# Kernel optimization log

Hardware: AMD Instinct MI355X
Metric: run time of the kernel (lower is better)

Reference implementation:

```python
import jax, jax.numpy as jnp
import numpy as np

NUM_HEADS = 8


def _cross_attn(q, k, v, mask, scale):
    # q: [N,H,Dh], k/v: [M,H,Dh], mask: [N,M] bool (True = same graph)
    scores = jnp.einsum('nhd,mhd->hnm', q, k) * scale          # [H,N,M]
    scores = jnp.where(mask[None, :, :], scores, jnp.float32(-1e9))
    attn = jax.nn.softmax(scores, axis=-1)                      # [H,N,M]
    return jnp.einsum('hnm,mhd->nhd', attn, v)                  # [N,H,Dh]


def setup_inputs() -> dict:
    key = jax.random.key(0)
    ks = jax.random.split(key, 12)
    Nd, Nr, Dd, Dr, Hd, B = 2048, 4096, 128, 128, 256, 64
    drug_nodes = jax.random.normal(ks[0], (Nd, Dd), jnp.float32)
    rna_nodes = jax.random.normal(ks[1], (Nr, Dr), jnp.float32)
    drug_batch_idx = jnp.sort(jax.random.randint(ks[2], (Nd,), 0, B, dtype=jnp.int32))
    rna_batch_idx = jnp.sort(jax.random.randint(ks[3], (Nr,), 0, B, dtype=jnp.int32))
    def lin(k, fan_in, fan_out):
        bound = 1.0 / np.sqrt(fan_in)
        return jax.random.uniform(k, (fan_in, fan_out), jnp.float32, -bound, bound)
    Wq_d = lin(ks[4], Dd, Hd)
    Wk_r = lin(ks[5], Dr, Hd)
    Wv_r = lin(ks[6], Dr, Hd)
    Wo_d = lin(ks[7], Hd, Dd)
    bo_d = jnp.zeros((Dd,), jnp.float32)
    Wq_r = lin(ks[8], Dr, Hd)
    Wk_d = lin(ks[9], Dd, Hd)
    Wv_d = lin(ks[10], Dd, Hd)
    Wo_r = lin(ks[11], Hd, Dr)
    bo_r = jnp.zeros((Dr,), jnp.float32)
    return dict(drug_nodes=drug_nodes, rna_nodes=rna_nodes,
                Wq_d=Wq_d, Wk_r=Wk_r, Wv_r=Wv_r, Wo_d=Wo_d, bo_d=bo_d,
                Wq_r=Wq_r, Wk_d=Wk_d, Wv_d=Wv_d, Wo_r=Wo_r, bo_r=bo_r,
                drug_batch_idx=drug_batch_idx, rna_batch_idx=rna_batch_idx)


def reference(drug_nodes, rna_nodes, Wq_d, Wk_r, Wv_r, Wo_d, bo_d,
              Wq_r, Wk_d, Wv_d, Wo_r, bo_r, drug_batch_idx, rna_batch_idx):
    H = NUM_HEADS
    Nd, Nr = drug_nodes.shape[0], rna_nodes.shape[0]
    head_dim = Wq_d.shape[1] // H
    scale = jnp.float32(head_dim) ** -0.5
    # block-diagonal batch mask: True where drug atom and RNA node share a graph
    mask = drug_batch_idx[:, None] == rna_batch_idx[None, :]   # [Nd, Nr]

    # drug queries attend to RNA keys/values
    q_d = (drug_nodes @ Wq_d).reshape(Nd, H, head_dim)
    k_r = (rna_nodes @ Wk_r).reshape(Nr, H, head_dim)
    v_r = (rna_nodes @ Wv_r).reshape(Nr, H, head_dim)
    ctx_drug = _cross_attn(q_d, k_r, v_r, mask, scale).reshape(Nd, H * head_dim)
    ctx_drug = ctx_drug @ Wo_d + bo_d                           # [Nd, drug_dim]

    # RNA queries attend to drug keys/values
    q_r = (rna_nodes @ Wq_r).reshape(Nr, H, head_dim)
    k_d = (drug_nodes @ Wk_d).reshape(Nd, H, head_dim)
    v_d = (drug_nodes @ Wv_d).reshape(Nd, H, head_dim)
    ctx_rna = _cross_attn(q_r, k_d, v_d, mask.T, scale).reshape(Nr, H * head_dim)
    ctx_rna = ctx_rna @ Wo_r + bo_r                             # [Nr, rna_dim]

    return (ctx_drug, ctx_rna)
```

## Files before the change

kernel.cpp:

```cpp
#include <hip/hip_runtime.h>
#include <math.h>

#define NHEADS 8
#define DH 32
#define NB 64
#define PR 8
#define OPR 8
#define KT 112

__global__ __launch_bounds__(256) void proj_all(
    const float* __restrict__ Xd, const float* __restrict__ Xr,
    int Nd, int Nr, float scale,
    const float* __restrict__ Wq_d, const float* __restrict__ Wk_d, const float* __restrict__ Wv_d,
    const float* __restrict__ Wq_r, const float* __restrict__ Wk_r, const float* __restrict__ Wv_r,
    float* __restrict__ Qd, float* __restrict__ Kd, float* __restrict__ Vd,
    float* __restrict__ Qr, float* __restrict__ Kr, float* __restrict__ Vr,
    const int* __restrict__ didx, const int* __restrict__ ridx,
    int* __restrict__ dstart, int* __restrict__ rstart)
{
    int t = threadIdx.x;
    if (blockIdx.x == 0) {
        if (t <= NB) {
            int lo = 0, hi = Nd;
            while (lo < hi) { int mid = (lo + hi) >> 1; if (didx[mid] < t) lo = mid + 1; else hi = mid; }
            dstart[t] = lo;
        } else if (t >= 128 && t <= 128 + NB) {
            int v = t - 128, lo = 0, hi = Nr;
            while (lo < hi) { int mid = (lo + hi) >> 1; if (ridx[mid] < v) lo = mid + 1; else hi = mid; }
            rstart[v] = lo;
        }
    }

    int ndc = Nd / PR;
    int chunk = blockIdx.x;
    const float *X, *Wq, *Wk, *Wv;
    float *Q, *K, *V;
    int N, row0;
    if (chunk < ndc) {
        X = Xd; N = Nd; row0 = chunk * PR;
        Wq = Wq_d; Wk = Wk_d; Wv = Wv_d; Q = Qd; K = Kd; V = Vd;
    } else {
        X = Xr; N = Nr; row0 = (chunk - ndc) * PR;
        Wq = Wq_r; Wk = Wk_r; Wv = Wv_r; Q = Qr; K = Kr; V = Vr;
    }

    __shared__ float xs[PR][128];
    ((float4*)xs)[t] = ((const float4*)(X + (size_t)row0 * 128))[t];
    __syncthreads();

    float aq[PR], ak[PR], av[PR];
#pragma unroll
    for (int r = 0; r < PR; ++r) { aq[r] = 0.f; ak[r] = 0.f; av[r] = 0.f; }

    for (int k = 0; k < 128; ++k) {
        float wq = Wq[k * 256 + t];
        float wk = Wk[k * 256 + t];
        float wv = Wv[k * 256 + t];
#pragma unroll
        for (int r = 0; r < PR; ++r) {
            float x = xs[r][k];
            aq[r] = fmaf(x, wq, aq[r]);
            ak[r] = fmaf(x, wk, ak[r]);
            av[r] = fmaf(x, wv, av[r]);
        }
    }

    int h = t >> 5, d = t & 31;
#pragma unroll
    for (int r = 0; r < PR; ++r) {
        size_t o = ((size_t)h * N + (row0 + r)) * DH + d;
        Q[o] = aq[r] * scale;
        K[o] = ak[r];
        V[o] = av[r];
    }
}

__global__ __launch_bounds__(512) void attn_batch(
    const float* __restrict__ Qd, const float* __restrict__ Kd, const float* __restrict__ Vd,
    const float* __restrict__ Qr, const float* __restrict__ Kr, const float* __restrict__ Vr,
    const int* __restrict__ dstart, const int* __restrict__ rstart,
    int Nd, int Nr, float* __restrict__ Cd, float* __restrict__ Cr)
{
    __shared__ float Kl[KT * 33];
    __shared__ float Vl[KT * 33];
    __shared__ float2 p2[8][KT];

    int b = blockIdx.x, h = blockIdx.y, side = blockIdx.z;
    const float *Q, *K, *V; const int *qst, *kst; float* C; int Nq, Nk;
    if (side == 0) { Q = Qd; K = Kr; V = Vr; qst = dstart; kst = rstart; Nq = Nd; Nk = Nr; C = Cd; }
    else           { Q = Qr; K = Kd; V = Vd; qst = rstart; kst = dstart; Nq = Nr; Nk = Nd; C = Cr; }

    int q0 = qst[b], nq = qst[b + 1] - q0;
    int k0 = kst[b], nk = kst[b + 1] - k0;
    if (nq <= 0 || nk <= 0) return;

    const float* Kb = K + ((size_t)h * Nk + k0) * DH;
    const float* Vb = V + ((size_t)h * Nk + k0) * DH;

    int t = threadIdx.x;
    int nst = nk < KT ? nk : KT;
    for (int j = t >> 5; j < nst; j += 16) {
        int e = t & 31;
        Kl[j * 33 + e] = Kb[(size_t)j * DH + e];
        Vl[j * 33 + e] = Vb[(size_t)j * DH + e];
    }
    __syncthreads();

    int wid = t >> 6, lane = t & 63;
    int d = lane & 31, j2 = lane >> 5;

    for (int r0 = q0 + 2 * wid; r0 < q0 + nq; r0 += 16) {
        int r1 = r0 + 1;
        bool has1 = r1 < q0 + nq;
        int r1c = has1 ? r1 : r0;

        float qa[DH], qb[DH];
        {
            const float* pa = Q + ((size_t)h * Nq + r0) * DH;
            const float* pb = Q + ((size_t)h * Nq + r1c) * DH;
#pragma unroll
            for (int e4 = 0; e4 < 8; ++e4) {
                float4 va4 = ((const float4*)pa)[e4];
                float4 vb4 = ((const float4*)pb)[e4];
                qa[4*e4+0]=va4.x; qa[4*e4+1]=va4.y; qa[4*e4+2]=va4.z; qa[4*e4+3]=va4.w;
                qb[4*e4+0]=vb4.x; qb[4*e4+1]=vb4.y; qb[4*e4+2]=vb4.z; qb[4*e4+3]=vb4.w;
            }
        }

        float sa0 = 0.f, sb0 = 0.f, sa1 = 0.f, sb1 = 0.f;
#pragma unroll
        for (int e = 0; e < DH; ++e) {
            float ka = Kl[lane * 33 + e];
            float kb = Kl[(64 + lane) * 33 + e];
            sa0 = fmaf(qa[e], ka, sa0);
            sa1 = fmaf(qb[e], ka, sa1);
            sb0 = fmaf(qa[e], kb, sb0);
            sb1 = fmaf(qb[e], kb, sb1);
        }
        bool va = lane < nst, vb = 64 + lane < nst;
        float pa0 = va ? __expf(sa0) : 0.f;
        float pa1 = va ? __expf(sa1) : 0.f;
        float pb0 = vb ? __expf(sb0) : 0.f;
        float pb1 = vb ? __expf(sb1) : 0.f;

        float l0 = pa0 + pb0, l1 = pa1 + pb1;
#pragma unroll
        for (int off = 32; off >= 1; off >>= 1) {
            l0 += __shfl_xor(l0, off);
            l1 += __shfl_xor(l1, off);
        }

        p2[wid][lane] = make_float2(pa0, pa1);
        if (vb) p2[wid][64 + lane] = make_float2(pb0, pb1);
        asm volatile("s_waitcnt lgkmcnt(0)" ::: "memory");

        float o0 = 0.f, o1 = 0.f;
#pragma unroll 8
        for (int jj = j2; jj < nst; jj += 2) {
            float2 p = p2[wid][jj];
            float vv = Vl[jj * 33 + d];
            o0 = fmaf(p.x, vv, o0);
            o1 = fmaf(p.y, vv, o1);
        }

        for (int c0 = KT; c0 < nk; c0 += 64) {
            int j = c0 + lane;
            bool val = j < nk;
            int jc = val ? j : nk - 1;
            float s0t = 0.f, s1t = 0.f;
#pragma unroll
            for (int e = 0; e < DH; ++e) {
                float kv = Kb[(size_t)jc * DH + e];
                s0t = fmaf(qa[e], kv, s0t);
                s1t = fmaf(qb[e], kv, s1t);
            }
            float pt0 = val ? __expf(s0t) : 0.f;
            float pt1 = val ? __expf(s1t) : 0.f;
            float a0 = pt0, a1 = pt1;
#pragma unroll
            for (int off = 32; off >= 1; off >>= 1) {
                a0 += __shfl_xor(a0, off);
                a1 += __shfl_xor(a1, off);
            }
            l0 += a0; l1 += a1;
            p2[wid][lane] = make_float2(pt0, pt1);
            asm volatile("s_waitcnt lgkmcnt(0)" ::: "memory");
            int cend = (nk - c0) < 64 ? (nk - c0) : 64;
            for (int jj = j2; jj < cend; jj += 2) {
                float2 p = p2[wid][jj];
                float vv = Vb[(size_t)(c0 + jj) * DH + d];
                o0 = fmaf(p.x, vv, o0);
                o1 = fmaf(p.y, vv, o1);
            }
        }

        o0 += __shfl_xor(o0, 32);
        o1 += __shfl_xor(o1, 32);
        if (lane < DH) {
            C[(size_t)r0 * (NHEADS * DH) + h * DH + d] = o0 / l0;
            if (has1)
                C[(size_t)r1 * (NHEADS * DH) + h * DH + d] = o1 / l1;
        }
    }
}

__global__ __launch_bounds__(256) void outproj_all(
    const float* __restrict__ Cd, const float* __restrict__ Cr,
    const float* __restrict__ Wo_d, const float* __restrict__ bo_d,
    const float* __restrict__ Wo_r, const float* __restrict__ bo_r,
    int Nd, int Nr, float* __restrict__ out)
{
    int blk = blockIdx.x, ndb = Nd / OPR;
    const float *ctx, *Wo, *bo;
    float* o;
    if (blk < ndb) {
        int row0 = blk * OPR;
        ctx = Cd + (size_t)row0 * 256; Wo = Wo_d; bo = bo_d;
        o = out + (size_t)row0 * 128;
    } else {
        int rl = (blk - ndb) * OPR;
        ctx = Cr + (size_t)rl * 256; Wo = Wo_r; bo = bo_r;
        o = out + (size_t)(Nd + rl) * 128;
    }

    __shared__ float cs[OPR][256];
    int t = threadIdx.x;
#pragma unroll
    for (int i = 0; i < 2; ++i)
        ((float4*)cs)[t + i * 256] = ((const float4*)ctx)[t + i * 256];
    __syncthreads();

    int c = t & 127, rh = t >> 7;
    float bias = bo[c];
    float acc[4];
#pragma unroll
    for (int r = 0; r < 4; ++r) acc[r] = bias;

    for (int k = 0; k < 256; ++k) {
        float w = Wo[k * 128 + c];
#pragma unroll
        for (int r = 0; r < 4; ++r)
            acc[r] = fmaf(cs[rh * 4 + r][k], w, acc[r]);
    }
#pragma unroll
    for (int r = 0; r < 4; ++r)
        o[(size_t)(rh * 4 + r) * 128 + c] = acc[r];
}

extern "C" void kernel_launch(void* const* d_in, const int* in_sizes, int n_in,
                              void* d_out, int out_size, void* d_ws, size_t ws_size,
                              hipStream_t stream)
{
    const float* drug = (const float*)d_in[0];
    const float* rna  = (const float*)d_in[1];
    const float* Wq_d = (const float*)d_in[2];
    const float* Wk_r = (const float*)d_in[3];
    const float* Wv_r = (const float*)d_in[4];
    const float* Wo_d = (const float*)d_in[5];
    const float* bo_d = (const float*)d_in[6];
    const float* Wq_r = (const float*)d_in[7];
    const float* Wk_d = (const float*)d_in[8];
    const float* Wv_d = (const float*)d_in[9];
    const float* Wo_r = (const float*)d_in[10];
    const float* bo_r = (const float*)d_in[11];
    const int* didx = (const int*)d_in[12];
    const int* ridx = (const int*)d_in[13];
    int Nd = in_sizes[12], Nr = in_sizes[13];

    float* ws = (float*)d_ws;
    size_t SD = (size_t)Nd * 256, SR = (size_t)Nr * 256;
    float* Qd = ws;        float* Kd = Qd + SD;   float* Vd = Kd + SD;
    float* Qr = Vd + SD;   float* Kr = Qr + SR;   float* Vr = Kr + SR;
    float* Cd = Vr + SR;   float* Cr = Cd + SD;
    int* dstart = (int*)(Cr + SR);
    int* rstart = dstart + (NB + 1);

    float* out = (float*)d_out;
    const float scale = 0.17677669529663689f;

    int nblk = Nd / PR + Nr / PR;
    proj_all<<<nblk, 256, 0, stream>>>(drug, rna, Nd, Nr, scale,
                                       Wq_d, Wk_d, Wv_d, Wq_r, Wk_r, Wv_r,
                                       Qd, Kd, Vd, Qr, Kr, Vr,
                                       didx, ridx, dstart, rstart);
    attn_batch<<<dim3(NB, NHEADS, 2), 512, 0, stream>>>(
        Qd, Kd, Vd, Qr, Kr, Vr, dstart, rstart, Nd, Nr, Cd, Cr);
    outproj_all<<<Nd / OPR + Nr / OPR, 256, 0, stream>>>(
        Cd, Cr, Wo_d, bo_d, Wo_r, bo_r, Nd, Nr, out);
}
```

Before: 73.36 us.

## Process four query rows per wave in attention and double output-projection rows

```diff
diff --git a/kernel.cpp b/kernel.cpp
--- a/kernel.cpp
+++ b/kernel.cpp
@@ -5,7 +5,7 @@
 #define DH 32
 #define NB 64
 #define PR 8
-#define OPR 8
+#define OPR 16
 #define KT 112
 
 __global__ __launch_bounds__(256) void proj_all(
@@ -75,7 +75,7 @@
     }
 }
 
-__global__ __launch_bounds__(512) void attn_batch(
+__global__ __launch_bounds__(512, 4) void attn_batch(
     const float* __restrict__ Qd, const float* __restrict__ Kd, const float* __restrict__ Vd,
     const float* __restrict__ Qr, const float* __restrict__ Kr, const float* __restrict__ Vr,
     const int* __restrict__ dstart, const int* __restrict__ rstart,
@@ -83,7 +83,7 @@
 {
     __shared__ float Kl[KT * 33];
     __shared__ float Vl[KT * 33];
-    __shared__ float2 p2[8][KT];
+    __shared__ float4 p4[8][128];
 
     int b = blockIdx.x, h = blockIdx.y, side = blockIdx.z;
     const float *Q, *K, *V; const int *qst, *kst; float* C; int Nq, Nk;
@@ -108,98 +108,125 @@
 
     int wid = t >> 6, lane = t & 63;
     int d = lane & 31, j2 = lane >> 5;
-
-    for (int r0 = q0 + 2 * wid; r0 < q0 + nq; r0 += 16) {
-        int r1 = r0 + 1;
-        bool has1 = r1 < q0 + nq;
-        int r1c = has1 ? r1 : r0;
-
-        float qa[DH], qb[DH];
-        {
-            const float* pa = Q + ((size_t)h * Nq + r0) * DH;
-            const float* pb = Q + ((size_t)h * Nq + r1c) * DH;
-#pragma unroll
-            for (int e4 = 0; e4 < 8; ++e4) {
-                float4 va4 = ((const float4*)pa)[e4];
-                float4 vb4 = ((const float4*)pb)[e4];
-                qa[4*e4+0]=va4.x; qa[4*e4+1]=va4.y; qa[4*e4+2]=va4.z; qa[4*e4+3]=va4.w;
-                qb[4*e4+0]=vb4.x; qb[4*e4+1]=vb4.y; qb[4*e4+2]=vb4.z; qb[4*e4+3]=vb4.w;
-            }
-        }
-
-        float sa0 = 0.f, sb0 = 0.f, sa1 = 0.f, sb1 = 0.f;
-#pragma unroll
-        for (int e = 0; e < DH; ++e) {
-            float ka = Kl[lane * 33 + e];
-            float kb = Kl[(64 + lane) * 33 + e];
-            sa0 = fmaf(qa[e], ka, sa0);
-            sa1 = fmaf(qb[e], ka, sa1);
-            sb0 = fmaf(qa[e], kb, sb0);
-            sb1 = fmaf(qb[e], kb, sb1);
-        }
+    int rend = q0 + nq;
+
+    for (int r0 = q0 + 4 * wid; r0 < rend; r0 += 32) {
+        int rmax = rend - 1;
+        int r1 = r0 + 1 < rmax ? r0 + 1 : rmax;
+        int r2 = r0 + 2 < rmax ? r0 + 2 : rmax;
+        int r3 = r0 + 3 < rmax ? r0 + 3 : rmax;
+
+        const float* qp0 = Q + ((size_t)h * Nq + r0) * DH;
+        const float* qp1 = Q + ((size_t)h * Nq + r1) * DH;
+        const float* qp2 = Q + ((size_t)h * Nq + r2) * DH;
+        const float* qp3 = Q + ((size_t)h * Nq + r3) * DH;
+
+        float s00 = 0.f, s01 = 0.f, s10 = 0.f, s11 = 0.f;
+        float s20 = 0.f, s21 = 0.f, s30 = 0.f, s31 = 0.f;
+
+#pragma unroll
+        for (int p = 0; p < 2; ++p) {
+            float q0r[16], q1r[16], q2r[16], q3r[16];
+#pragma unroll
+            for (int e4 = 0; e4 < 4; ++e4) {
+                float4 a = ((const float4*)qp0)[p * 4 + e4];
+                float4 bq = ((const float4*)qp1)[p * 4 + e4];
+                float4 c = ((const float4*)qp2)[p * 4 + e4];
+                float4 dq = ((const float4*)qp3)[p * 4 + e4];
+                q0r[4*e4+0]=a.x;  q0r[4*e4+1]=a.y;  q0r[4*e4+2]=a.z;  q0r[4*e4+3]=a.w;
+                q1r[4*e4+0]=bq.x; q1r[4*e4+1]=bq.y; q1r[4*e4+2]=bq.z; q1r[4*e4+3]=bq.w;
+                q2r[4*e4+0]=c.x;  q2r[4*e4+1]=c.y;  q2r[4*e4+2]=c.z;  q2r[4*e4+3]=c.w;
+                q3r[4*e4+0]=dq.x; q3r[4*e4+1]=dq.y; q3r[4*e4+2]=dq.z; q3r[4*e4+3]=dq.w;
+            }
+#pragma unroll
+            for (int e = 0; e < 16; ++e) {
+                float ka = Kl[lane * 33 + p * 16 + e];
+                float kb = Kl[(64 + lane) * 33 + p * 16 + e];
+                s00 = fmaf(q0r[e], ka, s00); s01 = fmaf(q0r[e], kb, s01);
+                s10 = fmaf(q1r[e], ka, s10); s11 = fmaf(q1r[e], kb, s11);
+                s20 = fmaf(q2r[e], ka, s20); s21 = fmaf(q2r[e], kb, s21);
+                s30 = fmaf(q3r[e], ka, s30); s31 = fmaf(q3r[e], kb, s31);
+            }
+        }
+
         bool va = lane < nst, vb = 64 + lane < nst;
-        float pa0 = va ? __expf(sa0) : 0.f;
-        float pa1 = va ? __expf(sa1) : 0.f;
-        float pb0 = vb ? __expf(sb0) : 0.f;
-        float pb1 = vb ? __expf(sb1) : 0.f;
-
-        float l0 = pa0 + pb0, l1 = pa1 + pb1;
+        float pa0 = va ? __expf(s00) : 0.f, pb0 = vb ? __expf(s01) : 0.f;
+        float pa1 = va ? __expf(s10) : 0.f, pb1 = vb ? __expf(s11) : 0.f;
+        float pa2 = va ? __expf(s20) : 0.f, pb2 = vb ? __expf(s21) : 0.f;
+        float pa3 = va ? __expf(s30) : 0.f, pb3 = vb ? __expf(s31) : 0.f;
+
+        float l0 = pa0 + pb0, l1 = pa1 + pb1, l2 = pa2 + pb2, l3 = pa3 + pb3;
 #pragma unroll
         for (int off = 32; off >= 1; off >>= 1) {
             l0 += __shfl_xor(l0, off);
             l1 += __shfl_xor(l1, off);
-        }
-
-        p2[wid][lane] = make_float2(pa0, pa1);
-        if (vb) p2[wid][64 + lane] = make_float2(pb0, pb1);
+            l2 += __shfl_xor(l2, off);
+            l3 += __shfl_xor(l3, off);
+        }
+
+        p4[wid][lane]      = make_float4(pa0, pa1, pa2, pa3);
+        p4[wid][64 + lane] = make_float4(pb0, pb1, pb2, pb3);
         asm volatile("s_waitcnt lgkmcnt(0)" ::: "memory");
 
-        float o0 = 0.f, o1 = 0.f;
+        float o0 = 0.f, o1 = 0.f, o2 = 0.f, o3 = 0.f;
 #pragma unroll 8
         for (int jj = j2; jj < nst; jj += 2) {
-            float2 p = p2[wid][jj];
+            float4 p = p4[wid][jj];
             float vv = Vl[jj * 33 + d];
             o0 = fmaf(p.x, vv, o0);
             o1 = fmaf(p.y, vv, o1);
+            o2 = fmaf(p.z, vv, o2);
+            o3 = fmaf(p.w, vv, o3);
         }
 
         for (int c0 = KT; c0 < nk; c0 += 64) {
             int j = c0 + lane;
             bool val = j < nk;
             int jc = val ? j : nk - 1;
-            float s0t = 0.f, s1t = 0.f;
+            float t0 = 0.f, t1 = 0.f, t2 = 0.f, t3 = 0.f;
 #pragma unroll
             for (int e = 0; e < DH; ++e) {
                 float kv = Kb[(size_t)jc * DH + e];
-                s0t = fmaf(qa[e], kv, s0t);
-                s1t = fmaf(qb[e], kv, s1t);
-            }
-            float pt0 = val ? __expf(s0t) : 0.f;
-            float pt1 = val ? __expf(s1t) : 0.f;
-            float a0 = pt0, a1 = pt1;
+                t0 = fmaf(qp0[e], kv, t0);
+                t1 = fmaf(qp1[e], kv, t1);
+                t2 = fmaf(qp2[e], kv, t2);
+                t3 = fmaf(qp3[e], kv, t3);
+            }
+            float u0 = val ? __expf(t0) : 0.f;
+            float u1 = val ? __expf(t1) : 0.f;
+            float u2 = val ? __expf(t2) : 0.f;
+            float u3 = val ? __expf(t3) : 0.f;
+            float a0 = u0, a1 = u1, a2 = u2, a3 = u3;
 #pragma unroll
             for (int off = 32; off >= 1; off >>= 1) {
                 a0 += __shfl_xor(a0, off);
                 a1 += __shfl_xor(a1, off);
-            }
-            l0 += a0; l1 += a1;
-            p2[wid][lane] = make_float2(pt0, pt1);
+                a2 += __shfl_xor(a2, off);
+                a3 += __shfl_xor(a3, off);
+            }
+            l0 += a0; l1 += a1; l2 += a2; l3 += a3;
+            p4[wid][lane] = make_float4(u0, u1, u2, u3);
             asm volatile("s_waitcnt lgkmcnt(0)" ::: "memory");
             int cend = (nk - c0) < 64 ? (nk - c0) : 64;
             for (int jj = j2; jj < cend; jj += 2) {
-                float2 p = p2[wid][jj];
+                float4 p = p4[wid][jj];
                 float vv = Vb[(size_t)(c0 + jj) * DH + d];
                 o0 = fmaf(p.x, vv, o0);
                 o1 = fmaf(p.y, vv, o1);
+                o2 = fmaf(p.z, vv, o2);
+                o3 = fmaf(p.w, vv, o3);
             }
         }
 
         o0 += __shfl_xor(o0, 32);
         o1 += __shfl_xor(o1, 32);
+        o2 += __shfl_xor(o2, 32);
+        o3 += __shfl_xor(o3, 32);
         if (lane < DH) {
             C[(size_t)r0 * (NHEADS * DH) + h * DH + d] = o0 / l0;
-            if (has1)
-                C[(size_t)r1 * (NHEADS * DH) + h * DH + d] = o1 / l1;
+            if (r0 + 1 < rend) C[(size_t)(r0 + 1) * (NHEADS * DH) + h * DH + d] = o1 / l1;
+            if (r0 + 2 < rend) C[(size_t)(r0 + 2) * (NHEADS * DH) + h * DH + d] = o2 / l2;
+            if (r0 + 3 < rend) C[(size_t)(r0 + 3) * (NHEADS * DH) + h * DH + d] = o3 / l3;
         }
     }
 }
@@ -226,25 +253,25 @@
     __shared__ float cs[OPR][256];
     int t = threadIdx.x;
 #pragma unroll
-    for (int i = 0; i < 2; ++i)
+    for (int i = 0; i < 4; ++i)
         ((float4*)cs)[t + i * 256] = ((const float4*)ctx)[t + i * 256];
     __syncthreads();
 
     int c = t & 127, rh = t >> 7;
     float bias = bo[c];
-    float acc[4];
-#pragma unroll
-    for (int r = 0; r < 4; ++r) acc[r] = bias;
+    float acc[8];
+#pragma unroll
+    for (int r = 0; r < 8; ++r) acc[r] = bias;
 
     for (int k = 0; k < 256; ++k) {
         float w = Wo[k * 128 + c];
 #pragma unroll
-        for (int r = 0; r < 4; ++r)
-            acc[r] = fmaf(cs[rh * 4 + r][k], w, acc[r]);
-    }
-#pragma unroll
-    for (int r = 0; r < 4; ++r)
-        o[(size_t)(rh * 4 + r) * 128 + c] = acc[r];
+        for (int r = 0; r < 8; ++r)
+            acc[r] = fmaf(cs[rh * 8 + r][k], w, acc[r]);
+    }
+#pragma unroll
+    for (int r = 0; r < 8; ++r)
+        o[(size_t)(rh * 8 + r) * 128 + c] = acc[r];
 }
 
 extern "C" void kernel_launch(void* const* d_in, const int* in_sizes, int n_in,
```

New measurement: 81.75 us. 1.11x slower.
